# Kernel optimization log

Measured on AMD Instinct MI355X. Metric: run time of the kernel, lower is better.

The kernel has to match this reference:

```python
import jax, jax.numpy as jnp
import numpy as np

B, C, H, W = 4, 512, 64, 64
CA = C // 2  # attention hidden channels


def _conv1x1(x, w):
    # w: [O, I], x: [B, I, H, W]
    return jnp.einsum('oi,bihw->bohw', w, x)


def _conv3x3(x, w, b):
    y = jax.lax.conv_general_dilated(x, w, (1, 1), 'SAME',
                                     dimension_numbers=('NCHW', 'OIHW', 'NCHW'))
    return y + b[None, :, None, None]


def _scan_dir(x, w, b, axis, reverse):
    # IRNN recurrence along `axis`: prev = relu(prev * w + b + x_t), per-channel w,b.
    # The boundary position (first in scan order after un-flipping) stays zero,
    # matching the torch code which never writes it.
    xs = jnp.moveaxis(x, axis, 0)          # [L, B, C, other]
    if reverse:
        xs = xs[::-1]
    wb = w.reshape(1, -1, 1)
    bb = b.reshape(1, -1, 1)

    def step(prev, xt):
        new = jax.nn.relu(prev * wb + bb + xt)
        return new, new

    init = jax.nn.relu(xs[0])
    _, ys = jax.lax.scan(step, init, xs[1:])
    ys = jnp.concatenate([jnp.zeros_like(ys[:1]), ys], axis=0)
    if reverse:
        ys = ys[::-1]
    return jnp.moveaxis(ys, 0, axis)


def _irnn(x, wu, wr, wd, wl, bu, br, bd, bl):
    up = _scan_dir(x, wu, bu, 2, True)     # scans from bottom row upward
    right = _scan_dir(x, wr, br, 3, False)
    down = _scan_dir(x, wd, bd, 2, False)
    left = _scan_dir(x, wl, bl, 3, True)
    return up, right, down, left


def setup_inputs() -> dict:
    key = jax.random.key(0)
    ks = jax.random.split(key, 32)

    def n(k, shape, scale):
        return jax.random.normal(k, shape, jnp.float32) * scale

    inp = {
        'x': n(ks[0], (B, C, H, W), 1.0),
        # Attention: conv3x3(C->C/2)+b, conv3x3(C/2->C/2)+b, conv1x1(C/2->4)+b
        'a_w1': n(ks[1], (CA, C, 3, 3), (C * 9) ** -0.5),
        'a_b1': n(ks[2], (CA,), 0.02),
        'a_w2': n(ks[3], (CA, CA, 3, 3), (CA * 9) ** -0.5),
        'a_b2': n(ks[4], (CA,), 0.02),
        'a_w3': n(ks[5], (4, CA, 1, 1), CA ** -0.5),
        'a_b3': n(ks[6], (4,), 0.02),
        'cin_w': n(ks[7], (C, C), C ** -0.5),   # conv_in 1x1, bias=False
        'c2_w': n(ks[8], (C, 4 * C), (4 * C) ** -0.5),
        'c3_w': n(ks[9], (C, 4 * C), (4 * C) ** -0.5),
    }
    # IRNN per-channel recurrence weights (alpha=1.0 init) and biases
    i = 10
    for tag in ('i1', 'i2'):
        for d in ('u', 'r', 'd', 'l'):
            inp[f'{tag}_w{d}'] = jnp.ones((C,), jnp.float32)
            inp[f'{tag}_b{d}'] = n(ks[i], (C,), 0.05)
            i += 1
    return inp


def reference(x, a_w1, a_b1, a_w2, a_b2, a_w3, a_b3, cin_w,
              i1_wu, i1_bu, i1_wr, i1_br, i1_wd, i1_bd, i1_wl, i1_bl,
              c2_w,
              i2_wu, i2_bu, i2_wr, i2_br, i2_wd, i2_bd, i2_wl, i2_bl,
              c3_w):
    # Attention branch — computed but NEVER applied: the original torch code
    # uses out-of-place .mul() and discards the result (faithful reproduction).
    a = jax.nn.relu(_conv3x3(x, a_w1, a_b1))
    a = jax.nn.relu(_conv3x3(a, a_w2, a_b2))
    _weight = jax.nn.sigmoid(_conv1x1(a, a_w3[:, :, 0, 0]) + a_b3[None, :, None, None])

    out = _conv1x1(x, cin_w)
    u, r, d, l = _irnn(out, i1_wu, i1_wr, i1_wd, i1_wl, i1_bu, i1_br, i1_bd, i1_bl)
    out = jnp.concatenate([u, r, d, l], axis=1)   # [B, 4C, H, W]
    out = _conv1x1(out, c2_w)
    u, r, d, l = _irnn(out, i2_wu, i2_wr, i2_wd, i2_wl, i2_bu, i2_br, i2_bd, i2_bl)
    out = jnp.concatenate([u, r, d, l], axis=1)
    out = jax.nn.relu(_conv1x1(out, c3_w))
    return out
```

## Files before the change

kernel.cpp:

```cpp
#include <hip/hip_runtime.h>
#include <stdint.h>

#define NB 4
#define CB 512
#define HH 64
#define WW 64
#define HW 4096
#define C4 2048
#define PTOT (NB*HW)

typedef float  f32x4  __attribute__((ext_vector_type(4)));
typedef short  bf16x8 __attribute__((ext_vector_type(8)));

__device__ __forceinline__ float relu_f(float v){ return v > 0.f ? v : 0.f; }

__device__ __forceinline__ float bf2f(unsigned short u){
    union { uint32_t i; float f; } v; v.i = ((uint32_t)u) << 16; return v.f;
}
__device__ __forceinline__ unsigned short f2bf(float f){
    union { float f; uint32_t i; } v; v.f = f;
    uint32_t r = v.i + 0x7FFFu + ((v.i >> 16) & 1u);
    return (unsigned short)(r >> 16);
}

__device__ __forceinline__ void gload16(const void* g, void* l){
    __builtin_amdgcn_global_load_lds(
        (const __attribute__((address_space(1))) uint32_t*)g,
        (__attribute__((address_space(3))) uint32_t*)l, 16, 0, 0);
}

__global__ __launch_bounds__(256) void cast3_f32_bf16(
    const float* __restrict__ a, unsigned short* __restrict__ oa,
    const float* __restrict__ b, unsigned short* __restrict__ ob,
    const float* __restrict__ c, unsigned short* __restrict__ oc)
{
    int i = blockIdx.x * 256 + threadIdx.x;
    const float* src; unsigned short* dst; int j;
    if (i < 65536)        { src = a; dst = oa; j = i; }
    else if (i < 327680)  { src = b; dst = ob; j = i - 65536; }
    else                  { src = c; dst = oc; j = i - 327680; }
    float4 v = ((const float4*)src)[j];
    ushort4 o;
    o.x = f2bf(v.x); o.y = f2bf(v.y); o.z = f2bf(v.z); o.w = f2bf(v.w);
    ((ushort4*)dst)[j] = o;
}

__global__ __launch_bounds__(256) void transpose_cast_x(
    const float* __restrict__ x, unsigned short* __restrict__ xT)
{
    __shared__ unsigned short tile[64][72];
    const int b  = blockIdx.z;
    const int p0 = blockIdx.x * 64;
    const int c0 = blockIdx.y * 64;
    const int t  = threadIdx.x;

    const int pl = (t & 15) * 4;
    const int cl = t >> 4;
    const float* src = x + ((size_t)b * CB + c0) * HW + p0;
    #pragma unroll
    for (int r = 0; r < 4; r++) {
        int c = cl + r * 16;
        float4 v = *(const float4*)(src + (size_t)c * HW + pl);
        tile[pl + 0][c] = f2bf(v.x);
        tile[pl + 1][c] = f2bf(v.y);
        tile[pl + 2][c] = f2bf(v.z);
        tile[pl + 3][c] = f2bf(v.w);
    }
    __syncthreads();
    unsigned short* dst = xT + ((size_t)b * HW + p0) * CB + c0;
    const int cl2 = (t & 15) * 4;
    const int pl2 = t >> 4;
    #pragma unroll
    for (int r = 0; r < 4; r++) {
        int p = pl2 + r * 16;
        ushort4 o = *(ushort4*)&tile[p][cl2];
        *(ushort4*)(dst + (size_t)p * CB + cl2) = o;
    }
}

template<int K, int OUTMODE>
__global__ __launch_bounds__(256) void gemm_cl(
    const unsigned short* __restrict__ A,
    const unsigned short* __restrict__ Bw,
    void* __restrict__ out)
{
    __shared__ __align__(16) char lds[65536];

    const int t    = threadIdx.x;
    const int lane = t & 63;
    const int wid  = t >> 6;
    const int p0   = blockIdx.x * 128;
    const int o0   = blockIdx.y * 128;

    const int l15 = lane & 15;
    const int l4  = lane >> 4;
    const int wp  = (wid & 1) * 64;
    const int wo  = (wid >> 1) * 64;
    const int rowA = wp + l15;
    const int rowB = wo + l15;
    const int swzA = (rowA & 7) << 4;
    const int swzB = (rowB & 7) << 4;

    f32x4 acc[4][4];
    #pragma unroll
    for (int m = 0; m < 4; m++)
        #pragma unroll
        for (int n = 0; n < 4; n++) acc[m][n] = (f32x4)0.f;

    const int srow  = t >> 3;
    const int scolb = (t & 7) * 16;

    auto STAGE = [&](int k0, char* base) {
        #pragma unroll
        for (int q = 0; q < 4; q++) {
            const int row = q * 32 + srow;
            const int kk  = k0 + ((scolb ^ ((row & 7) << 4)) >> 1);
            gload16(A  + (size_t)(p0 + row) * K + kk, base +         q * 4096 + wid * 1024);
            gload16(Bw + (size_t)(o0 + row) * K + kk, base + 16384 + q * 4096 + wid * 1024);
        }
    };
    auto COMPUTE = [&](const char* base) {
        const char* cA = base;
        const char* cB = base + 16384;
        #pragma unroll
        for (int kh = 0; kh < 2; kh++) {
            const int colb = kh * 64 + l4 * 16;
            bf16x8 a[4], b[4];
            #pragma unroll
            for (int m = 0; m < 4; m++)
                a[m] = *(const bf16x8*)(cA + (rowA + m * 16) * 128 + (colb ^ swzA));
            #pragma unroll
            for (int n = 0; n < 4; n++)
                b[n] = *(const bf16x8*)(cB + (rowB + n * 16) * 128 + (colb ^ swzB));
            __builtin_amdgcn_s_setprio(1);
            #pragma unroll
            for (int m = 0; m < 4; m++)
                #pragma unroll
                for (int n = 0; n < 4; n++)
                    acc[m][n] = __builtin_amdgcn_mfma_f32_16x16x32_bf16(
                                    a[m], b[n], acc[m][n], 0, 0, 0);
            __builtin_amdgcn_s_setprio(0);
        }
    };

    const int NT = K / 64;
    STAGE(0, lds);
    __syncthreads();
    #pragma unroll 2
    for (int tt = 0; tt < NT - 1; ++tt) {
        char* cbase = lds + ((tt & 1) ? 32768 : 0);
        char* nbase = lds + ((tt & 1) ? 0 : 32768);
        STAGE((tt + 1) * 64, nbase);
        COMPUTE(cbase);
        __syncthreads();
    }
    COMPUTE(lds + (((NT - 1) & 1) ? 32768 : 0));

    if (OUTMODE == 0) {
        unsigned short* op = (unsigned short*)out;
        #pragma unroll
        for (int m = 0; m < 4; m++)
            #pragma unroll
            for (int r = 0; r < 4; r++) {
                const int p = p0 + wp + m * 16 + l4 * 4 + r;
                #pragma unroll
                for (int n = 0; n < 4; n++) {
                    const int o = wo + n * 16 + l15 + o0;
                    op[(size_t)p * CB + o] = f2bf(acc[m][n][r]);
                }
            }
    } else {
        __syncthreads();
        float (*tl)[132] = (float(*)[132])lds;
        const int bb   = p0 >> 12;
        const int phw0 = p0 & (HW - 1);
        #pragma unroll
        for (int half = 0; half < 2; half++) {
            if ((wid >> 1) == half) {
                #pragma unroll
                for (int n = 0; n < 4; n++)
                    #pragma unroll
                    for (int m = 0; m < 4; m++)
                        #pragma unroll
                        for (int r = 0; r < 4; r++)
                            tl[n * 16 + l15][wp + m * 16 + l4 * 4 + r] = acc[m][n][r];
            }
            __syncthreads();
            const int orow = t >> 2;
            const int pseg = (t & 3) * 32;
            float* dst = (float*)out +
                ((size_t)(bb * CB + o0 + half * 64 + orow)) * HW + phw0 + pseg;
            #pragma unroll
            for (int j = 0; j < 8; j++) {
                float4 v = *(float4*)&tl[orow][pseg + j * 4];
                v.x = relu_f(v.x); v.y = relu_f(v.y); v.z = relu_f(v.z); v.w = relu_f(v.w);
                *(float4*)(dst + j * 4) = v;
            }
            __syncthreads();
        }
    }
}

__global__ __launch_bounds__(256) void irnn_fused(
    const unsigned short* __restrict__ in, unsigned short* __restrict__ outc,
    const float* __restrict__ wu, const float* __restrict__ bu,
    const float* __restrict__ wr, const float* __restrict__ br,
    const float* __restrict__ wd, const float* __restrict__ bd,
    const float* __restrict__ wl, const float* __restrict__ bl)
{
    const int dir = blockIdx.y;
    const float* wv; const float* bv; int pstep, rev;
    if      (dir == 0) { wv = wu; bv = bu; pstep = 64; rev = 1; }
    else if (dir == 1) { wv = wr; bv = br; pstep = 1;  rev = 0; }
    else if (dir == 2) { wv = wd; bv = bd; pstep = 64; rev = 0; }
    else               { wv = wl; bv = bl; pstep = 1;  rev = 1; }
    const int dirOff = dir * 512;

    const int idx = blockIdx.x * 256 + threadIdx.x;
    const int c = idx & 511;
    const int f = (idx >> 9) & 63;
    const int b = idx >> 15;
    const int fbase = (pstep == 64) ? f : f * 64;

    const float wc = wv[c], bc = bv[c];
    const int t0 = rev ? 63 : 0;
    const int dp = rev ? -pstep : pstep;
    const int istep = dp * CB;
    const int ostep = dp * C4;

    const unsigned short* ip = in   + ((size_t)b * HW + fbase + (size_t)t0 * pstep) * CB + c;
    unsigned short*       op = outc + ((size_t)b * HW + fbase + (size_t)t0 * pstep) * C4 + dirOff + c;

    float s = relu_f(bf2f(ip[0]));
    op[0] = 0;

    unsigned short v0 = ip[1*istep], v1 = ip[2*istep], v2 = ip[3*istep], v3 = ip[4*istep],
                   v4 = ip[5*istep], v5 = ip[6*istep], v6 = ip[7*istep], v7 = ip[8*istep];

#define DO(kk, vv) { s = relu_f(fmaf(s, wc, bc + bf2f(vv))); op[(kk)*ostep] = f2bf(s); }
    for (int g = 0; g < 6; ++g) {
        const int k0 = 1 + 8 * g;
        DO(k0+0, v0); v0 = ip[(k0+ 8)*istep];
        DO(k0+1, v1); v1 = ip[(k0+ 9)*istep];
        DO(k0+2, v2); v2 = ip[(k0+10)*istep];
        DO(k0+3, v3); v3 = ip[(k0+11)*istep];
        DO(k0+4, v4); v4 = ip[(k0+12)*istep];
        DO(k0+5, v5); v5 = ip[(k0+13)*istep];
        DO(k0+6, v6); v6 = ip[(k0+14)*istep];
        DO(k0+7, v7); v7 = ip[(k0+15)*istep];
    }
    DO(49, v0); v0 = ip[57*istep];
    DO(50, v1); v1 = ip[58*istep];
    DO(51, v2); v2 = ip[59*istep];
    DO(52, v3); v3 = ip[60*istep];
    DO(53, v4); v4 = ip[61*istep];
    DO(54, v5); v5 = ip[62*istep];
    DO(55, v6); v6 = ip[63*istep];
    DO(56, v7);
    DO(57, v0); DO(58, v1); DO(59, v2); DO(60, v3);
    DO(61, v4); DO(62, v5); DO(63, v6);
#undef DO
}

extern "C" void kernel_launch(void* const* d_in, const int* in_sizes, int n_in,
                              void* d_out, int out_size, void* d_ws, size_t ws_size,
                              hipStream_t stream) {
    const float* x     = (const float*)d_in[0];
    const float* cin_w = (const float*)d_in[7];
    const float* c2_w  = (const float*)d_in[8];
    const float* c3_w  = (const float*)d_in[9];
    const float* i1_wu = (const float*)d_in[10];
    const float* i1_bu = (const float*)d_in[11];
    const float* i1_wr = (const float*)d_in[12];
    const float* i1_br = (const float*)d_in[13];
    const float* i1_wd = (const float*)d_in[14];
    const float* i1_bd = (const float*)d_in[15];
    const float* i1_wl = (const float*)d_in[16];
    const float* i1_bl = (const float*)d_in[17];
    const float* i2_wu = (const float*)d_in[18];
    const float* i2_bu = (const float*)d_in[19];
    const float* i2_wr = (const float*)d_in[20];
    const float* i2_br = (const float*)d_in[21];
    const float* i2_wd = (const float*)d_in[22];
    const float* i2_bd = (const float*)d_in[23];
    const float* i2_wl = (const float*)d_in[24];
    const float* i2_bl = (const float*)d_in[25];

    char* ws = (char*)d_ws;
    unsigned short* xT     = (unsigned short*)(ws);
    unsigned short* concat = (unsigned short*)(ws + (size_t)16 * 1024 * 1024);
    unsigned short* mid    = (unsigned short*)(ws + (size_t)80 * 1024 * 1024);
    unsigned short* wA     = (unsigned short*)(ws + (size_t)96 * 1024 * 1024);
    unsigned short* wB     = (unsigned short*)(wA + 512 * 512);
    unsigned short* wC     = (unsigned short*)(wB + 512 * 2048);

    cast3_f32_bf16<<<2304, 256, 0, stream>>>(cin_w, wA, c2_w, wB, c3_w, wC);

    transpose_cast_x<<<dim3(HW/64, CB/64, NB), 256, 0, stream>>>(x, xT);

    dim3 ggrid(PTOT/128, 4);
    dim3 sgrid(512, 4);

    gemm_cl<512, 0><<<ggrid, 256, 0, stream>>>(xT, wA, mid);

    irnn_fused<<<sgrid, 256, 0, stream>>>(mid, concat,
        i1_wu, i1_bu, i1_wr, i1_br, i1_wd, i1_bd, i1_wl, i1_bl);

    gemm_cl<2048, 0><<<ggrid, 256, 0, stream>>>(concat, wB, mid);

    irnn_fused<<<sgrid, 256, 0, stream>>>(mid, concat,
        i2_wu, i2_bu, i2_wr, i2_br, i2_wd, i2_bd, i2_wl, i2_bl);

    gemm_cl<2048, 1><<<ggrid, 256, 0, stream>>>(concat, wC, d_out);
}
```

Before: 144.0 us.

## Use 256x128 GEMM tiles with 8 waves and triple-buffered LDS pipeline

Restructures the bf16 MFMA GEMM to 512-thread blocks computing 256x128 tiles, with a three-stage LDS ring buffer that prefetches two K-steps ahead. Global-load staging is interleaved into four MFMA phases, with explicit waitcnt, barriers and scheduling fences. The aim is to hide global-memory latency and raise operand reuse per block. In exchange it uses 144KB of dynamic LDS, limiting residency to one block per CU, and the fine-grained barriers may stall waves.

```diff
diff --git a/kernel.cpp b/kernel.cpp
--- a/kernel.cpp
+++ b/kernel.cpp
@@ -79,27 +79,24 @@
 }
 
 template<int K, int OUTMODE>
-__global__ __launch_bounds__(256) void gemm_cl(
+__global__ __launch_bounds__(512, 2) void gemm_cl(
     const unsigned short* __restrict__ A,
     const unsigned short* __restrict__ Bw,
     void* __restrict__ out)
 {
-    __shared__ __align__(16) char lds[65536];
+    extern __shared__ __align__(16) char lds[];
 
     const int t    = threadIdx.x;
     const int lane = t & 63;
     const int wid  = t >> 6;
-    const int p0   = blockIdx.x * 128;
+    const int p0   = blockIdx.x * 256;
     const int o0   = blockIdx.y * 128;
 
     const int l15 = lane & 15;
     const int l4  = lane >> 4;
-    const int wp  = (wid & 1) * 64;
-    const int wo  = (wid >> 1) * 64;
-    const int rowA = wp + l15;
-    const int rowB = wo + l15;
-    const int swzA = (rowA & 7) << 4;
-    const int swzB = (rowB & 7) << 4;
+    const int m0  = (wid >> 1) * 64;
+    const int n0  = (wid & 1) * 64;
+    const int swz = (l15 & 7) << 4;
 
     f32x4 acc[4][4];
     #pragma unroll
@@ -107,54 +104,82 @@
         #pragma unroll
         for (int n = 0; n < 4; n++) acc[m][n] = (f32x4)0.f;
 
-    const int srow  = t >> 3;
-    const int scolb = (t & 7) * 16;
-
-    auto STAGE = [&](int k0, char* base) {
-        #pragma unroll
-        for (int q = 0; q < 4; q++) {
-            const int row = q * 32 + srow;
-            const int kk  = k0 + ((scolb ^ ((row & 7) << 4)) >> 1);
-            gload16(A  + (size_t)(p0 + row) * K + kk, base +         q * 4096 + wid * 1024);
-            gload16(Bw + (size_t)(o0 + row) * K + kk, base + 16384 + q * 4096 + wid * 1024);
+    const int sr  = lane >> 3;
+    const int scb = (lane & 7) * 16;
+    const int skk = (scb ^ (sr << 4)) >> 1;
+
+    auto STAGE_A = [&](int k0, int half, char* buf) {
+        #pragma unroll
+        for (int j = 0; j < 2; ++j) {
+            const int r = half * 128 + j * 64 + wid * 8 + sr;
+            gload16(A + (size_t)(p0 + r) * K + k0 + skk,
+                    buf + half * 16384 + j * 8192 + wid * 1024);
         }
     };
-    auto COMPUTE = [&](const char* base) {
-        const char* cA = base;
-        const char* cB = base + 16384;
-        #pragma unroll
-        for (int kh = 0; kh < 2; kh++) {
-            const int colb = kh * 64 + l4 * 16;
-            bf16x8 a[4], b[4];
-            #pragma unroll
-            for (int m = 0; m < 4; m++)
-                a[m] = *(const bf16x8*)(cA + (rowA + m * 16) * 128 + (colb ^ swzA));
-            #pragma unroll
-            for (int n = 0; n < 4; n++)
-                b[n] = *(const bf16x8*)(cB + (rowB + n * 16) * 128 + (colb ^ swzB));
-            __builtin_amdgcn_s_setprio(1);
-            #pragma unroll
-            for (int m = 0; m < 4; m++)
-                #pragma unroll
-                for (int n = 0; n < 4; n++)
-                    acc[m][n] = __builtin_amdgcn_mfma_f32_16x16x32_bf16(
-                                    a[m], b[n], acc[m][n], 0, 0, 0);
-            __builtin_amdgcn_s_setprio(0);
+    auto STAGE_B = [&](int k0, char* buf) {
+        #pragma unroll
+        for (int j = 0; j < 2; ++j) {
+            const int r = j * 64 + wid * 8 + sr;
+            gload16(Bw + (size_t)(o0 + r) * K + k0 + skk,
+                    buf + 32768 + j * 8192 + wid * 1024);
         }
     };
 
+    char* buf0 = lds;
+    char* buf1 = lds + 49152;
+    char* buf2 = lds + 98304;
+
+    STAGE_A(0, 0, buf0); STAGE_A(0, 1, buf0); STAGE_B(0, buf0);
+    STAGE_A(64, 0, buf1); STAGE_A(64, 1, buf1); STAGE_B(64, buf1);
+
+    char* cur = buf0; char* nxt = buf1; char* fut = buf2;
     const int NT = K / 64;
-    STAGE(0, lds);
-    __syncthreads();
-    #pragma unroll 2
-    for (int tt = 0; tt < NT - 1; ++tt) {
-        char* cbase = lds + ((tt & 1) ? 32768 : 0);
-        char* nbase = lds + ((tt & 1) ? 0 : 32768);
-        STAGE((tt + 1) * 64, nbase);
-        COMPUTE(cbase);
-        __syncthreads();
-    }
-    COMPUTE(lds + (((NT - 1) & 1) ? 32768 : 0));
+
+#define PH(khv, mhv, STCODE)                                                   \
+    {                                                                          \
+        const int colb = (khv) * 64 + l4 * 16;                                 \
+        af0 = *(const bf16x8*)(cur + (m0 + (2*(mhv)  )*16 + l15)*128 + (colb ^ swz)); \
+        af1 = *(const bf16x8*)(cur + (m0 + (2*(mhv)+1)*16 + l15)*128 + (colb ^ swz)); \
+        if ((mhv) == 0) {                                                      \
+            _Pragma("unroll")                                                  \
+            for (int nn = 0; nn < 4; ++nn)                                     \
+                bfr[nn] = *(const bf16x8*)(cur + 32768 +                       \
+                           (n0 + nn*16 + l15)*128 + (colb ^ swz));             \
+        }                                                                      \
+        STCODE;                                                                \
+        __builtin_amdgcn_s_barrier();                                          \
+        asm volatile("s_waitcnt lgkmcnt(0)" ::: "memory");                     \
+        __builtin_amdgcn_sched_barrier(0);                                     \
+        __builtin_amdgcn_s_setprio(1);                                         \
+        _Pragma("unroll")                                                      \
+        for (int nn = 0; nn < 4; ++nn) {                                       \
+            acc[2*(mhv)  ][nn] = __builtin_amdgcn_mfma_f32_16x16x32_bf16(      \
+                                    af0, bfr[nn], acc[2*(mhv)  ][nn], 0, 0, 0);\
+            acc[2*(mhv)+1][nn] = __builtin_amdgcn_mfma_f32_16x16x32_bf16(      \
+                                    af1, bfr[nn], acc[2*(mhv)+1][nn], 0, 0, 0);\
+        }                                                                      \
+        __builtin_amdgcn_s_setprio(0);                                         \
+        __builtin_amdgcn_sched_barrier(0);                                     \
+        __builtin_amdgcn_s_barrier();                                          \
+    }
+
+    for (int tt = 0; tt < NT; ++tt) {
+        if (tt < NT - 1) asm volatile("s_waitcnt vmcnt(6)" ::: "memory");
+        else             asm volatile("s_waitcnt vmcnt(0)" ::: "memory");
+        __builtin_amdgcn_s_barrier();
+
+        const int  k2 = (tt + 2) * 64;
+        const bool st = (tt + 2 < NT);
+        bf16x8 bfr[4], af0, af1;
+
+        PH(0, 0, { if (st) STAGE_A(k2, 0, fut); })
+        PH(0, 1, { if (st) STAGE_A(k2, 1, fut); })
+        PH(1, 0, { if (st) STAGE_B(k2, fut);    })
+        PH(1, 1, { })
+
+        char* tmp = cur; cur = nxt; nxt = fut; fut = tmp;
+    }
+#undef PH
 
     if (OUTMODE == 0) {
         unsigned short* op = (unsigned short*)out;
@@ -162,41 +187,34 @@
         for (int m = 0; m < 4; m++)
             #pragma unroll
             for (int r = 0; r < 4; r++) {
-                const int p = p0 + wp + m * 16 + l4 * 4 + r;
+                const int p = p0 + m0 + m * 16 + l4 * 4 + r;
                 #pragma unroll
                 for (int n = 0; n < 4; n++) {
-                    const int o = wo + n * 16 + l15 + o0;
+                    const int o = o0 + n0 + n * 16 + l15;
                     op[(size_t)p * CB + o] = f2bf(acc[m][n][r]);
                 }
             }
     } else {
         __syncthreads();
-        float (*tl)[132] = (float(*)[132])lds;
+        float (*tl)[260] = (float(*)[260])lds;
+        #pragma unroll
+        for (int n = 0; n < 4; n++)
+            #pragma unroll
+            for (int m = 0; m < 4; m++)
+                #pragma unroll
+                for (int r = 0; r < 4; r++)
+                    tl[n0 + n * 16 + l15][m0 + m * 16 + l4 * 4 + r] = acc[m][n][r];
+        __syncthreads();
         const int bb   = p0 >> 12;
         const int phw0 = p0 & (HW - 1);
-        #pragma unroll
-        for (int half = 0; half < 2; half++) {
-            if ((wid >> 1) == half) {
-                #pragma unroll
-                for (int n = 0; n < 4; n++)
-                    #pragma unroll
-                    for (int m = 0; m < 4; m++)
-                        #pragma unroll
-                        for (int r = 0; r < 4; r++)
-                            tl[n * 16 + l15][wp + m * 16 + l4 * 4 + r] = acc[m][n][r];
-            }
-            __syncthreads();
-            const int orow = t >> 2;
-            const int pseg = (t & 3) * 32;
-            float* dst = (float*)out +
-                ((size_t)(bb * CB + o0 + half * 64 + orow)) * HW + phw0 + pseg;
-            #pragma unroll
-            for (int j = 0; j < 8; j++) {
-                float4 v = *(float4*)&tl[orow][pseg + j * 4];
-                v.x = relu_f(v.x); v.y = relu_f(v.y); v.z = relu_f(v.z); v.w = relu_f(v.w);
-                *(float4*)(dst + j * 4) = v;
-            }
-            __syncthreads();
+        const int orow = t >> 2;
+        const int pseg = (t & 3) * 64;
+        float* dst = (float*)out + ((size_t)(bb * CB + o0 + orow)) * HW + phw0 + pseg;
+        #pragma unroll
+        for (int j = 0; j < 16; j++) {
+            float4 v = *(float4*)&tl[orow][pseg + j * 4];
+            v.x = relu_f(v.x); v.y = relu_f(v.y); v.z = relu_f(v.z); v.w = relu_f(v.w);
+            *(float4*)(dst + j * 4) = v;
         }
     }
 }
@@ -295,21 +313,21 @@
     unsigned short* wC     = (unsigned short*)(wB + 512 * 2048);
 
     cast3_f32_bf16<<<2304, 256, 0, stream>>>(cin_w, wA, c2_w, wB, c3_w, wC);
-
     transpose_cast_x<<<dim3(HW/64, CB/64, NB), 256, 0, stream>>>(x, xT);
 
-    dim3 ggrid(PTOT/128, 4);
+    dim3 ggrid(PTOT/256, 4);
     dim3 sgrid(512, 4);
-
-    gemm_cl<512, 0><<<ggrid, 256, 0, stream>>>(xT, wA, mid);
+    const size_t GEMM_LDS = 147456;
+
+    gemm_cl<512, 0><<<ggrid, 512, GEMM_LDS, stream>>>(xT, wA, mid);
 
     irnn_fused<<<sgrid, 256, 0, stream>>>(mid, concat,
         i1_wu, i1_bu, i1_wr, i1_br, i1_wd, i1_bd, i1_wl, i1_bl);
 
-    gemm_cl<2048, 0><<<ggrid, 256, 0, stream>>>(concat, wB, mid);
+    gemm_cl<2048, 0><<<ggrid, 512, GEMM_LDS, stream>>>(concat, wB, mid);
 
     irnn_fused<<<sgrid, 256, 0, stream>>>(mid, concat,
         i2_wu, i2_bu, i2_wr, i2_br, i2_wd, i2_bd, i2_wl, i2_bl);
 
-    gemm_cl<2048, 1><<<ggrid, 256, 0, stream>>>(concat, wC, d_out);
-}
+    gemm_cl<2048, 1><<<ggrid, 512, GEMM_LDS, stream>>>(concat, wC, d_out);
+}
```

Result: slower. 168.3 us (+16.9%).
